# Performance work log

Hardware: AMD Instinct MI355X
Metric: run time of the kernel (lower is better)

Reference implementation:

```python
import jax, jax.numpy as jnp
import numpy as np


def setup_inputs() -> dict:
    key = jax.random.key(0)
    ks = jax.random.split(key, 8)
    B, C, H, W = 4, 256, 64, 64
    Ci = C // 8  # inter_channels = 32
    x = jax.random.normal(ks[0], (B, C, H, W), dtype=jnp.float32)
    # 1x1 conv weights stored as [out, in] matrices (kernel size 1)
    sq = 1.0 / np.sqrt(C)
    Wq = jax.random.uniform(ks[1], (Ci, C), jnp.float32, -sq, sq)
    bq = jax.random.uniform(ks[2], (Ci,), jnp.float32, -sq, sq)
    Wk = jax.random.uniform(ks[3], (Ci, C), jnp.float32, -sq, sq)
    bk = jax.random.uniform(ks[4], (Ci,), jnp.float32, -sq, sq)
    Wv = jax.random.uniform(ks[5], (C, C), jnp.float32, -sq, sq)
    bv = jax.random.uniform(ks[6], (C,), jnp.float32, -sq, sq)
    # torch initializes gamma to zeros; use a nonzero value so output depends on attention path
    gamma = jnp.array([0.5], dtype=jnp.float32)
    return {"x": x, "Wq": Wq, "bq": bq, "Wk": Wk, "bk": bk, "Wv": Wv, "bv": bv, "gamma": gamma}


def reference(x, Wq, bq, Wk, bk, Wv, bv, gamma):
    B, C, H, W = x.shape
    N = H * W
    xf = x.reshape(B, C, N)                        # [B, C, N]
    # 1x1 convs == channel-mixing matmuls
    q = jnp.einsum('oc,bcn->bon', Wq, xf) + bq[None, :, None]   # [B, Ci, N]
    k = jnp.einsum('oc,bcn->bon', Wk, xf) + bk[None, :, None]   # [B, Ci, N]
    v = jnp.einsum('oc,bcn->bon', Wv, xf) + bv[None, :, None]   # [B, C,  N]
    # energy[b, n, m] = sum_c q[b, c, n] * k[b, c, m]  (no scaling, per DANet)
    energy = jnp.einsum('bcn,bcm->bnm', q, k)      # [B, N, N]
    attention = jax.nn.softmax(energy, axis=-1)    # softmax over keys m
    # out[b, c, n] = sum_m v[b, c, m] * attention[b, n, m]
    out = jnp.einsum('bcm,bnm->bcn', v, attention)
    out = out.reshape(B, C, H, W)
    return gamma[0] * out + x
```

## Files before the change

kernel.cpp:

```cpp
#include <hip/hip_runtime.h>
#include <hip/hip_bf16.h>
#include <math.h>

typedef __bf16 bf16x8 __attribute__((ext_vector_type(8)));
typedef float  floatx4 __attribute__((ext_vector_type(4)));

#define MFMA(a, b, c) __builtin_amdgcn_mfma_f32_16x16x32_bf16((a), (b), (c), 0, 0, 0)

__device__ __forceinline__ unsigned short f2bf(float f) {
  union { float f; unsigned u; } v; v.f = f;
  unsigned r = v.u + 0x7FFFu + ((v.u >> 16) & 1u);
  return (unsigned short)(r >> 16);
}
__device__ __forceinline__ float bf2f(unsigned short u) {
  union { unsigned u; float f; } v; v.u = ((unsigned)u) << 16;
  return v.f;
}

__global__ __launch_bounds__(256) void k_wconv(const float* __restrict__ Wq,
                                               const float* __restrict__ Wk,
                                               const float* __restrict__ Wv,
                                               unsigned short* __restrict__ Wall) {
  int i = blockIdx.x * 256 + threadIdx.x;
  int o = i >> 8, c = i & 255;
  float v = (o < 32) ? Wq[o * 256 + c]
          : (o < 64) ? Wk[(o - 32) * 256 + c]
                     : Wv[(o - 64) * 256 + c];
  Wall[i] = f2bf(v);
}

__global__ __launch_bounds__(256) void k_xpose(const float* __restrict__ x,
                                               unsigned short* __restrict__ xT) {
  int bid = blockIdx.x;
  int b = bid >> 8, rem = bid & 255;
  int nb = rem >> 2, cb = rem & 3;
  int n0 = nb * 64, c0 = cb * 64;
  int tid = threadIdx.x;
  __shared__ alignas(16) unsigned short T[64][72];
#pragma unroll
  for (int i = 0; i < 4; ++i) {
    int idx = tid + 256 * i;
    int r = idx >> 4, g = idx & 15;
    float4 d = *(const float4*)(x + ((size_t)b * 256 + c0 + r) * 4096 + n0 + g * 4);
    T[g * 4 + 0][r] = f2bf(d.x);
    T[g * 4 + 1][r] = f2bf(d.y);
    T[g * 4 + 2][r] = f2bf(d.z);
    T[g * 4 + 3][r] = f2bf(d.w);
  }
  __syncthreads();
#pragma unroll
  for (int i = 0; i < 2; ++i) {
    int idx = tid + 256 * i;
    int j = idx >> 3, g = idx & 7;
    *(uint4*)(xT + ((size_t)b * 4096 + n0 + j) * 256 + c0 + g * 8) =
        *(const uint4*)&T[j][g * 8];
  }
}

__global__ __launch_bounds__(64, 4) void k_proj(const unsigned short* __restrict__ xT,
                                                const unsigned short* __restrict__ Wall,
                                                const float* __restrict__ bq,
                                                const float* __restrict__ bk,
                                                const float* __restrict__ bv,
                                                unsigned short* __restrict__ qkT,
                                                unsigned short* __restrict__ vbf) {
  int b = blockIdx.x >> 9;
  int m0 = ((blockIdx.x >> 1) & 255) * 16;
  int h = blockIdx.x & 1;
  int lane = threadIdx.x & 63;
  int l15 = lane & 15, quad = lane >> 4;

  floatx4 acc[10];
#pragma unroll
  for (int tt = 0; tt < 10; ++tt) acc[tt] = floatx4{0.f, 0.f, 0.f, 0.f};

  const unsigned short* arow = xT + ((size_t)b * 4096 + m0 + l15) * 256;
#pragma unroll
  for (int ks = 0; ks < 8; ++ks) {
    bf16x8 a = *(const bf16x8*)(arow + ks * 32 + quad * 8);
#pragma unroll
    for (int tt = 0; tt < 10; ++tt) {
      int gt = (tt < 2) ? (h * 2 + tt) : (4 + h * 8 + (tt - 2));
      bf16x8 w = *(const bf16x8*)(Wall + (size_t)(gt * 16 + l15) * 256 + ks * 32 + quad * 8);
      acc[tt] = MFMA(a, w, acc[tt]);
    }
  }
#pragma unroll
  for (int tt = 0; tt < 2; ++tt) {
    int o = (h * 2 + tt) * 16 + l15;
    float bias = (o < 32) ? bq[o] : bk[o - 32];
#pragma unroll
    for (int r = 0; r < 4; ++r) {
      int m = m0 + quad * 4 + r;
      qkT[((size_t)b * 4096 + m) * 64 + o] = f2bf(acc[tt][r] + bias);
    }
  }
  __shared__ alignas(16) unsigned short Os[128][24];
#pragma unroll
  for (int tt = 2; tt < 10; ++tt) {
    int lr = (tt - 2) * 16 + l15;
    int c = h * 128 + lr;
    float bias = bv[c];
#pragma unroll
    for (int r = 0; r < 4; ++r)
      Os[lr][quad * 4 + r] = f2bf(acc[tt][r] + bias);
  }
  __syncthreads();
#pragma unroll
  for (int i = 0; i < 4; ++i) {
    int idx = threadIdx.x + 64 * i;
    int r = idx >> 1, g = idx & 1;
    int c = h * 128 + r;
    *(uint4*)(vbf + ((size_t)b * 256 + c) * 4096 + m0 + g * 8) = *(const uint4*)&Os[r][g * 8];
  }
}

__global__ __launch_bounds__(256, 3) void k_attn(const unsigned short* __restrict__ qkT,
                                                 const unsigned short* __restrict__ vbf,
                                                 unsigned short* __restrict__ Obf,
                                                 float* __restrict__ lsum) {
  const int b = blockIdx.x >> 8;
  const int s = (blockIdx.x >> 6) & 3;
  const int q0 = (blockIdx.x & 63) * 64;
  const int tid = threadIdx.x;
  const int wave = tid >> 6, lane = tid & 63;
  const int l15 = lane & 15, quad = lane >> 4;

  __shared__ alignas(16) unsigned short Kl[2][64][40];
  __shared__ alignas(16) unsigned short Pl[4][16][72];

  bf16x8 aq = *(const bf16x8*)(qkT + ((size_t)b * 4096 + q0 + wave * 16 + l15) * 64 + quad * 8);

  floatx4 O[4][4];
#pragma unroll
  for (int qt = 0; qt < 4; ++qt)
#pragma unroll
    for (int nt = 0; nt < 4; ++nt) O[qt][nt] = floatx4{0.f, 0.f, 0.f, 0.f};

  float l_part = 0.f;
  const floatx4 zero4 = {0.f, 0.f, 0.f, 0.f};

  const unsigned short* vrow = vbf + ((size_t)b * 256 + wave * 64) * 4096;

  {
    int r = tid >> 2, g = tid & 3;
    uint4 d = *(const uint4*)(qkT + ((size_t)b * 4096 + s * 1024 + r) * 64 + 32 + g * 8);
    *(uint4*)&Kl[0][r][g * 8] = d;
  }
  __syncthreads();

  for (int it = 0; it < 16; ++it) {
    const int m0 = (s * 16 + it) * 64;
    const int buf = it & 1;

    bf16x8 vb[4][2];
#pragma unroll
    for (int nt = 0; nt < 4; ++nt)
#pragma unroll
      for (int kk = 0; kk < 2; ++kk)
        vb[nt][kk] = *(const bf16x8*)(vrow + (size_t)(nt * 16 + l15) * 4096 + m0 + kk * 32 + quad * 8);

    floatx4 st[4];
#pragma unroll
    for (int t = 0; t < 4; ++t) {
      bf16x8 kb = *(const bf16x8*)&Kl[buf][t * 16 + l15][quad * 8];
      st[t] = MFMA(kb, aq, zero4);
    }
#pragma unroll
    for (int t = 0; t < 4; ++t) {
      float p0 = __expf(st[t][0]);
      float p1 = __expf(st[t][1]);
      float p2 = __expf(st[t][2]);
      float p3 = __expf(st[t][3]);
      l_part += (p0 + p1) + (p2 + p3);
      ushort4 pk = make_ushort4(f2bf(p0), f2bf(p1), f2bf(p2), f2bf(p3));
      *(ushort4*)&Pl[wave][l15][t * 16 + quad * 4] = pk;
    }

    if (it < 15) {
      int r = tid >> 2, g = tid & 3;
      uint4 d = *(const uint4*)(qkT + ((size_t)b * 4096 + m0 + 64 + r) * 64 + 32 + g * 8);
      *(uint4*)&Kl[buf ^ 1][r][g * 8] = d;
    }
    __syncthreads();

#pragma unroll
    for (int qt = 0; qt < 4; ++qt) {
      bf16x8 pa0 = *(const bf16x8*)&Pl[qt][l15][quad * 8];
      bf16x8 pa1 = *(const bf16x8*)&Pl[qt][l15][32 + quad * 8];
#pragma unroll
      for (int nt = 0; nt < 4; ++nt) {
        O[qt][nt] = MFMA(pa0, vb[nt][0], O[qt][nt]);
        O[qt][nt] = MFMA(pa1, vb[nt][1], O[qt][nt]);
      }
    }
    __syncthreads();
  }

  float lt = l_part;
  lt += __shfl_xor(lt, 16);
  lt += __shfl_xor(lt, 32);
  if (quad == 0)
    lsum[((size_t)s * 4 + b) * 4096 + q0 + wave * 16 + l15] = lt;

#pragma unroll
  for (int nt = 0; nt < 4; ++nt) {
    size_t crow = (((size_t)s * 4 + b) * 256 + wave * 64 + nt * 16 + l15) * 4096;
#pragma unroll
    for (int qt = 0; qt < 4; ++qt) {
      ushort4 ok = make_ushort4(f2bf(O[qt][nt][0]), f2bf(O[qt][nt][1]),
                                f2bf(O[qt][nt][2]), f2bf(O[qt][nt][3]));
      *(ushort4*)(Obf + crow + q0 + qt * 16 + quad * 4) = ok;
    }
  }
}

__global__ __launch_bounds__(256) void k_merge(const unsigned short* __restrict__ Obf,
                                               const float* __restrict__ lsum,
                                               const float* __restrict__ x,
                                               const float* __restrict__ gma,
                                               float* __restrict__ out) {
  int t = blockIdx.x * 256 + threadIdx.x;
  int n4 = t & 1023;
  int c = (t >> 10) & 255;
  int b = t >> 18;
  int n = n4 << 2;
  size_t xa = (((size_t)b * 256 + c) << 12) + n;
  float4 xv = *(const float4*)(x + xa);
  float L0 = 0.f, L1 = 0.f, L2 = 0.f, L3 = 0.f;
  float o0 = 0.f, o1 = 0.f, o2 = 0.f, o3 = 0.f;
#pragma unroll
  for (int s = 0; s < 4; ++s) {
    float4 ls = *(const float4*)(lsum + (((size_t)s * 4 + b) << 12) + n);
    L0 += ls.x; L1 += ls.y; L2 += ls.z; L3 += ls.w;
    ushort4 ov = *(const ushort4*)(Obf + ((((size_t)s * 4 + b) * 256 + c) << 12) + n);
    o0 += bf2f(ov.x); o1 += bf2f(ov.y); o2 += bf2f(ov.z); o3 += bf2f(ov.w);
  }
  float g = gma[0];
  float4 r;
  r.x = xv.x + g * o0 / L0;
  r.y = xv.y + g * o1 / L1;
  r.z = xv.z + g * o2 / L2;
  r.w = xv.w + g * o3 / L3;
  *(float4*)(out + xa) = r;
}

extern "C" void kernel_launch(void* const* d_in, const int* in_sizes, int n_in,
                              void* d_out, int out_size, void* d_ws, size_t ws_size,
                              hipStream_t stream) {
  const float* x   = (const float*)d_in[0];
  const float* Wq  = (const float*)d_in[1];
  const float* bq  = (const float*)d_in[2];
  const float* Wk  = (const float*)d_in[3];
  const float* bk  = (const float*)d_in[4];
  const float* Wv  = (const float*)d_in[5];
  const float* bv  = (const float*)d_in[6];
  const float* gma = (const float*)d_in[7];
  float* out = (float*)d_out;

  unsigned short* qkT  = (unsigned short*)d_ws;
  unsigned short* vbf  = qkT + (size_t)4 * 4096 * 64;
  unsigned short* Wall = vbf + (size_t)4 * 256 * 4096;
  unsigned short* xT   = Wall + (size_t)320 * 256;
  unsigned short* Obf  = xT;
  float* lsum = (float*)(Obf + (size_t)4 * 4 * 256 * 4096);

  k_wconv<<<320, 256, 0, stream>>>(Wq, Wk, Wv, Wall);
  k_xpose<<<1024, 256, 0, stream>>>(x, xT);
  k_proj<<<2048, 64, 0, stream>>>(xT, Wall, bq, bk, bv, qkT, vbf);
  k_attn<<<1024, 256, 0, stream>>>(qkT, vbf, Obf, lsum);
  k_merge<<<4096, 256, 0, stream>>>(Obf, lsum, x, gma, out);
}
```

Baseline: 192.0 us.

## Rewrite attention kernel with single-wave 32x32 MFMA and register-resident P

Replaces the 4-wave attention workgroup, which staged K and P in shared memory, with one wave per workgroup. Each wave computes a 64-query by 128-channel tile using 32x32x16 bf16 MFMAs. The softmax probabilities are packed into bf16 and rearranged across lanes with permlane32_swap (or shuffles as a fallback), so they feed the PV MFMA straight from registers, with no LDS and no barriers. K and V are loaded directly from global memory, and the grid is remapped for locality. The cost is that each workgroup recomputes QK^T for both channel halves, and register pressure rises.

Result: slower. 203.6 us (+6.1%).

```diff
diff --git a/kernel.cpp b/kernel.cpp
--- a/kernel.cpp
+++ b/kernel.cpp
@@ -4,8 +4,11 @@
 
 typedef __bf16 bf16x8 __attribute__((ext_vector_type(8)));
 typedef float  floatx4 __attribute__((ext_vector_type(4)));
-
-#define MFMA(a, b, c) __builtin_amdgcn_mfma_f32_16x16x32_bf16((a), (b), (c), 0, 0, 0)
+typedef float  floatx16 __attribute__((ext_vector_type(16)));
+typedef unsigned u32x2 __attribute__((ext_vector_type(2)));
+
+#define MFMA(a, b, c)   __builtin_amdgcn_mfma_f32_16x16x32_bf16((a), (b), (c), 0, 0, 0)
+#define MFMA32(a, b, c) __builtin_amdgcn_mfma_f32_32x32x16_bf16((a), (b), (c), 0, 0, 0)
 
 __device__ __forceinline__ unsigned short f2bf(float f) {
   union { float f; unsigned u; } v; v.f = f;
@@ -15,6 +18,12 @@
 __device__ __forceinline__ float bf2f(unsigned short u) {
   union { unsigned u; float f; } v; v.u = ((unsigned)u) << 16;
   return v.f;
+}
+__device__ __forceinline__ unsigned pack2(float a, float b) {
+  __bf16 x = (__bf16)a, y = (__bf16)b;
+  unsigned short ux = __builtin_bit_cast(unsigned short, x);
+  unsigned short uy = __builtin_bit_cast(unsigned short, y);
+  return (unsigned)ux | ((unsigned)uy << 16);
 }
 
 __global__ __launch_bounds__(256) void k_wconv(const float* __restrict__ Wq,
@@ -115,104 +124,135 @@
   }
 }
 
-__global__ __launch_bounds__(256, 3) void k_attn(const unsigned short* __restrict__ qkT,
-                                                 const unsigned short* __restrict__ vbf,
-                                                 unsigned short* __restrict__ Obf,
-                                                 float* __restrict__ lsum) {
-  const int b = blockIdx.x >> 8;
-  const int s = (blockIdx.x >> 6) & 3;
-  const int q0 = (blockIdx.x & 63) * 64;
-  const int tid = threadIdx.x;
-  const int wave = tid >> 6, lane = tid & 63;
-  const int l15 = lane & 15, quad = lane >> 4;
-
-  __shared__ alignas(16) unsigned short Kl[2][64][40];
-  __shared__ alignas(16) unsigned short Pl[4][16][72];
-
-  bf16x8 aq = *(const bf16x8*)(qkT + ((size_t)b * 4096 + q0 + wave * 16 + l15) * 64 + quad * 8);
-
-  floatx4 O[4][4];
-#pragma unroll
-  for (int qt = 0; qt < 4; ++qt)
-#pragma unroll
-    for (int nt = 0; nt < 4; ++nt) O[qt][nt] = floatx4{0.f, 0.f, 0.f, 0.f};
-
-  float l_part = 0.f;
-  const floatx4 zero4 = {0.f, 0.f, 0.f, 0.f};
-
-  const unsigned short* vrow = vbf + ((size_t)b * 256 + wave * 64) * 4096;
-
+__device__ __forceinline__ void softmax_pack(floatx16 st, float& lp, bf16x8 (&pa)[2], int hi) {
+  float p[16];
+#pragma unroll
+  for (int r = 0; r < 16; ++r) p[r] = __expf(st[r]);
+  lp += (((p[0] + p[1]) + (p[2] + p[3])) + ((p[4] + p[5]) + (p[6] + p[7]))) +
+        (((p[8] + p[9]) + (p[10] + p[11])) + ((p[12] + p[13]) + (p[14] + p[15])));
+  unsigned d0[4], d1[4];
+#pragma unroll
+  for (int t = 0; t < 4; ++t) {
+    d0[t] = pack2(p[4 * t + 0], p[4 * t + 1]);
+    d1[t] = pack2(p[4 * t + 2], p[4 * t + 3]);
+  }
+#pragma unroll
+  for (int ks = 0; ks < 2; ++ks) {
+#if __has_builtin(__builtin_amdgcn_permlane32_swap)
+    (void)hi;
+    u32x2 r0 = __builtin_amdgcn_permlane32_swap(d0[2 * ks], d0[2 * ks + 1], false, false);
+    u32x2 r1 = __builtin_amdgcn_permlane32_swap(d1[2 * ks], d1[2 * ks + 1], false, false);
+    union { unsigned u[4]; bf16x8 v; } u;
+    u.u[0] = r0[0]; u.u[1] = r1[0]; u.u[2] = r0[1]; u.u[3] = r1[1];
+    pa[ks] = u.v;
+#else
+    unsigned s0 = hi ? d0[2 * ks] : d0[2 * ks + 1];
+    unsigned s1 = hi ? d1[2 * ks] : d1[2 * ks + 1];
+    unsigned o0 = (unsigned)__shfl_xor((int)s0, 32);
+    unsigned o1 = (unsigned)__shfl_xor((int)s1, 32);
+    union { unsigned u[4]; bf16x8 v; } u;
+    u.u[0] = hi ? o0 : d0[2 * ks];
+    u.u[1] = hi ? o1 : d1[2 * ks];
+    u.u[2] = hi ? d0[2 * ks + 1] : o0;
+    u.u[3] = hi ? d1[2 * ks + 1] : o1;
+    pa[ks] = u.v;
+#endif
+  }
+}
+
+__global__ __launch_bounds__(64, 2) void k_attn(const unsigned short* __restrict__ qkT,
+                                                const unsigned short* __restrict__ vbf,
+                                                unsigned short* __restrict__ Obf,
+                                                float* __restrict__ lsum) {
+  int wg = (blockIdx.x & 7) * 256 + (blockIdx.x >> 3);
+  const int qb = wg & 63;
+  const int g  = wg >> 6;
+  const int cw = g & 1;
+  const int s  = (g >> 1) & 3;
+  const int b  = g >> 3;
+  const int lane = threadIdx.x & 63;
+  const int l31 = lane & 31;
+  const int hi  = lane >> 5;
+  const int q0  = qb * 64;
+
+  const floatx16 z16 = {0.f, 0.f, 0.f, 0.f, 0.f, 0.f, 0.f, 0.f,
+                        0.f, 0.f, 0.f, 0.f, 0.f, 0.f, 0.f, 0.f};
+
+  bf16x8 qf[2][2];
   {
-    int r = tid >> 2, g = tid & 3;
-    uint4 d = *(const uint4*)(qkT + ((size_t)b * 4096 + s * 1024 + r) * 64 + 32 + g * 8);
-    *(uint4*)&Kl[0][r][g * 8] = d;
-  }
-  __syncthreads();
-
-  for (int it = 0; it < 16; ++it) {
-    const int m0 = (s * 16 + it) * 64;
-    const int buf = it & 1;
+    const unsigned short* qbase = qkT + ((size_t)b * 4096 + q0 + l31) * 64 + hi * 8;
+#pragma unroll
+    for (int qs2 = 0; qs2 < 2; ++qs2)
+#pragma unroll
+      for (int kh = 0; kh < 2; ++kh)
+        qf[qs2][kh] = *(const bf16x8*)(qbase + qs2 * 32 * 64 + kh * 16);
+  }
+
+  floatx16 acc[2][4];
+#pragma unroll
+  for (int i = 0; i < 2; ++i)
+#pragma unroll
+    for (int j = 0; j < 4; ++j) acc[i][j] = z16;
+
+  float lp0 = 0.f, lp1 = 0.f;
+
+  const unsigned short* krow = qkT + ((size_t)b * 4096 + s * 1024 + l31) * 64 + 32 + hi * 8;
+  const unsigned short* vrow = vbf + ((size_t)b * 256 + cw * 128 + l31) * 4096 + s * 1024 + hi * 8;
+
+  bf16x8 kf0 = *(const bf16x8*)krow;
+  bf16x8 kf1 = *(const bf16x8*)(krow + 16);
+
+  for (int it = 0; it < 32; ++it) {
+    floatx16 st0 = MFMA32(kf0, qf[0][0], z16);
+    st0 = MFMA32(kf1, qf[0][1], st0);
+    floatx16 st1 = MFMA32(kf0, qf[1][0], z16);
+    st1 = MFMA32(kf1, qf[1][1], st1);
 
     bf16x8 vb[4][2];
-#pragma unroll
-    for (int nt = 0; nt < 4; ++nt)
-#pragma unroll
-      for (int kk = 0; kk < 2; ++kk)
-        vb[nt][kk] = *(const bf16x8*)(vrow + (size_t)(nt * 16 + l15) * 4096 + m0 + kk * 32 + quad * 8);
-
-    floatx4 st[4];
-#pragma unroll
-    for (int t = 0; t < 4; ++t) {
-      bf16x8 kb = *(const bf16x8*)&Kl[buf][t * 16 + l15][quad * 8];
-      st[t] = MFMA(kb, aq, zero4);
-    }
-#pragma unroll
-    for (int t = 0; t < 4; ++t) {
-      float p0 = __expf(st[t][0]);
-      float p1 = __expf(st[t][1]);
-      float p2 = __expf(st[t][2]);
-      float p3 = __expf(st[t][3]);
-      l_part += (p0 + p1) + (p2 + p3);
-      ushort4 pk = make_ushort4(f2bf(p0), f2bf(p1), f2bf(p2), f2bf(p3));
-      *(ushort4*)&Pl[wave][l15][t * 16 + quad * 4] = pk;
-    }
-
-    if (it < 15) {
-      int r = tid >> 2, g = tid & 3;
-      uint4 d = *(const uint4*)(qkT + ((size_t)b * 4096 + m0 + 64 + r) * 64 + 32 + g * 8);
-      *(uint4*)&Kl[buf ^ 1][r][g * 8] = d;
-    }
-    __syncthreads();
-
-#pragma unroll
-    for (int qt = 0; qt < 4; ++qt) {
-      bf16x8 pa0 = *(const bf16x8*)&Pl[qt][l15][quad * 8];
-      bf16x8 pa1 = *(const bf16x8*)&Pl[qt][l15][32 + quad * 8];
-#pragma unroll
-      for (int nt = 0; nt < 4; ++nt) {
-        O[qt][nt] = MFMA(pa0, vb[nt][0], O[qt][nt]);
-        O[qt][nt] = MFMA(pa1, vb[nt][1], O[qt][nt]);
+    const unsigned short* vit = vrow + it * 32;
+#pragma unroll
+    for (int ct = 0; ct < 4; ++ct) {
+      vb[ct][0] = *(const bf16x8*)(vit + (size_t)ct * 32 * 4096);
+      vb[ct][1] = *(const bf16x8*)(vit + (size_t)ct * 32 * 4096 + 16);
+    }
+    const unsigned short* kn = krow + (size_t)((it + 1) & 31) * 2048;
+    kf0 = *(const bf16x8*)kn;
+    kf1 = *(const bf16x8*)(kn + 16);
+
+    bf16x8 pa[2][2];
+    softmax_pack(st0, lp0, pa[0], hi);
+    softmax_pack(st1, lp1, pa[1], hi);
+
+#pragma unroll
+    for (int ct = 0; ct < 4; ++ct) {
+      acc[0][ct] = MFMA32(pa[0][0], vb[ct][0], acc[0][ct]);
+      acc[1][ct] = MFMA32(pa[1][0], vb[ct][0], acc[1][ct]);
+      acc[0][ct] = MFMA32(pa[0][1], vb[ct][1], acc[0][ct]);
+      acc[1][ct] = MFMA32(pa[1][1], vb[ct][1], acc[1][ct]);
+    }
+  }
+
+  lp0 += __shfl_xor(lp0, 32);
+  lp1 += __shfl_xor(lp1, 32);
+  if (cw == 0) {
+    float lv = hi ? lp1 : lp0;
+    lsum[((size_t)s * 4 + b) * 4096 + q0 + hi * 32 + l31] = lv;
+  }
+#pragma unroll
+  for (int qs2 = 0; qs2 < 2; ++qs2)
+#pragma unroll
+    for (int ct = 0; ct < 4; ++ct) {
+      unsigned short* orow = Obf +
+          (((size_t)s * 4 + b) * 256 + cw * 128 + ct * 32 + l31) * 4096 +
+          q0 + qs2 * 32 + hi * 4;
+#pragma unroll
+      for (int gi = 0; gi < 4; ++gi) {
+        unsigned w0 = pack2(acc[qs2][ct][4 * gi + 0], acc[qs2][ct][4 * gi + 1]);
+        unsigned w1 = pack2(acc[qs2][ct][4 * gi + 2], acc[qs2][ct][4 * gi + 3]);
+        unsigned long long w = (unsigned long long)w0 | ((unsigned long long)w1 << 32);
+        *(unsigned long long*)(orow + 8 * gi) = w;
       }
     }
-    __syncthreads();
-  }
-
-  float lt = l_part;
-  lt += __shfl_xor(lt, 16);
-  lt += __shfl_xor(lt, 32);
-  if (quad == 0)
-    lsum[((size_t)s * 4 + b) * 4096 + q0 + wave * 16 + l15] = lt;
-
-#pragma unroll
-  for (int nt = 0; nt < 4; ++nt) {
-    size_t crow = (((size_t)s * 4 + b) * 256 + wave * 64 + nt * 16 + l15) * 4096;
-#pragma unroll
-    for (int qt = 0; qt < 4; ++qt) {
-      ushort4 ok = make_ushort4(f2bf(O[qt][nt][0]), f2bf(O[qt][nt][1]),
-                                f2bf(O[qt][nt][2]), f2bf(O[qt][nt][3]));
-      *(ushort4*)(Obf + crow + q0 + qt * 16 + quad * 4) = ok;
-    }
-  }
 }
 
 __global__ __launch_bounds__(256) void k_merge(const unsigned short* __restrict__ Obf,
@@ -268,6 +308,6 @@
   k_wconv<<<320, 256, 0, stream>>>(Wq, Wk, Wv, Wall);
   k_xpose<<<1024, 256, 0, stream>>>(x, xT);
   k_proj<<<2048, 64, 0, stream>>>(xT, Wall, bq, bk, bv, qkT, vbf);
-  k_attn<<<1024, 256, 0, stream>>>(qkT, vbf, Obf, lsum);
+  k_attn<<<2048, 64, 0, stream>>>(qkT, vbf, Obf, lsum);
   k_merge<<<4096, 256, 0, stream>>>(Obf, lsum, x, gma, out);
 }
```
